# Optimization experiments

Hardware: AMD Instinct MI355X
Metric: run time of the kernel (lower is better)

The kernel has to match this reference:

```python
import jax, jax.numpy as jnp
import numpy as np
from jax import lax
import math

D_MODEL = 768
EXPAND = 2
D_INNER = EXPAND * D_MODEL          # 1536 (= d_ssm since d_ssm=None)
D_STATE = 128
HEADDIM = 64
NHEADS = D_INNER // HEADDIM         # 24
D_CONV = 4
NGROUPS = 1
CONV_DIM = D_INNER + 2 * NGROUPS * D_STATE            # 1792
D_IN_PROJ = 2 * D_INNER + 2 * NGROUPS * D_STATE + NHEADS  # d_mlp = 0
BATCH, SEQLEN = 2, 2048
EPS = 1e-5


def setup_inputs() -> dict:
    key = jax.random.key(0)
    ks = jax.random.split(key, 8)
    u = jax.random.normal(ks[0], (BATCH, SEQLEN, D_MODEL), dtype=jnp.float32)
    in_proj_w = jax.random.normal(ks[1], (D_IN_PROJ, D_MODEL), dtype=jnp.float32) / math.sqrt(D_MODEL)
    conv_w = jax.random.uniform(ks[2], (CONV_DIM, D_CONV), dtype=jnp.float32, minval=-0.5, maxval=0.5)
    conv_b = jnp.zeros((CONV_DIM,), dtype=jnp.float32)
    # dt_bias = inverse-softplus of dt sampled log-uniform in [1e-3, 1e-1]
    dt = jnp.exp(jax.random.uniform(ks[3], (NHEADS,)) * (math.log(0.1) - math.log(0.001)) + math.log(0.001))
    dt_bias = dt + jnp.log(-jnp.expm1(-dt))
    A_log = jnp.log(jax.random.uniform(ks[4], (NHEADS,), minval=1.0, maxval=16.0))
    D = jnp.ones((NHEADS,), dtype=jnp.float32)
    norm_w = jnp.ones((D_INNER,), dtype=jnp.float32)
    out_proj_w = jax.random.normal(ks[5], (D_MODEL, D_INNER), dtype=jnp.float32) / math.sqrt(D_INNER)
    return {"u": u, "in_proj_w": in_proj_w, "conv_w": conv_w, "conv_b": conv_b,
            "dt_bias": dt_bias, "A_log": A_log, "D": D, "norm_w": norm_w,
            "out_proj_w": out_proj_w}


def _mamba2_forward(u, in_proj_w, conv_w, conv_b, dt_bias, A_log, D, norm_w, out_proj_w):
    b, l, _ = u.shape
    zxbcdt = u @ in_proj_w.T                                   # [b,l,D_IN_PROJ]
    z = zxbcdt[..., :D_INNER]                                  # [b,l,d_ssm]
    xBC = zxbcdt[..., D_INNER:D_INNER + CONV_DIM]              # [b,l,conv_dim]
    dt = zxbcdt[..., D_INNER + CONV_DIM:]                      # [b,l,h]

    # causal depthwise conv1d (pad d_conv-1 left == torch pad both + truncate tail)
    xBC_t = xBC.transpose(0, 2, 1)                             # [b,c,l]
    conv_out = lax.conv_general_dilated(
        xBC_t, conv_w[:, None, :], window_strides=(1,),
        padding=[(D_CONV - 1, 0)], feature_group_count=CONV_DIM,
        dimension_numbers=("NCH", "OIH", "NCH"))
    xBC = jax.nn.silu(conv_out + conv_b[None, :, None]).transpose(0, 2, 1)  # [b,l,c]

    x = xBC[..., :D_INNER].reshape(b, l, NHEADS, HEADDIM)      # [b,l,h,p]
    B = xBC[..., D_INNER:D_INNER + D_STATE]                    # [b,l,n]
    C = xBC[..., D_INNER + D_STATE:]                           # [b,l,n]

    A = -jnp.exp(A_log)                                        # [h]
    dt_dis = jax.nn.softplus(dt + dt_bias)                     # [b,l,h]  (dt_limit=(0,inf) -> no-op clamp)
    dA = jnp.exp(dt_dis * A)                                   # [b,l,h]

    def step(state, inp):
        dA_t, dt_t, B_t, x_t, C_t = inp
        dBx = jnp.einsum("bh,bn,bhp->bhpn", dt_t, B_t, x_t)    # [b,h,p,n]
        state = lax.stop_gradient(state * dA_t[:, :, None, None] + dBx)  # matches torch .detach()
        y_t = jnp.einsum("bhpn,bn->bhp", state, C_t)
        return state, y_t

    xs = (dA.transpose(1, 0, 2), dt_dis.transpose(1, 0, 2),
          B.transpose(1, 0, 2), x.transpose(1, 0, 2, 3), C.transpose(1, 0, 2))
    state0 = jnp.zeros((b, NHEADS, HEADDIM, D_STATE), dtype=u.dtype)
    _, ys = lax.scan(step, state0, xs)                         # [l,b,h,p]
    y = ys.transpose(1, 0, 2, 3) + x * D[None, None, :, None]  # D skip (per-head)
    y = y.reshape(b, l, D_INNER)

    # gated RMSNorm (norm_before_gate=False, group_size = d_ssm)
    yz = y * jax.nn.silu(z)
    y = yz * lax.rsqrt(jnp.mean(yz * yz, axis=-1, keepdims=True) + EPS) * norm_w

    return y @ out_proj_w.T                                    # [b,l,d_model]


def reference(u, in_proj_w, conv_w, conv_b, dt_bias, A_log, D, norm_w, out_proj_w):
    return _mamba2_forward(u, in_proj_w, conv_w, conv_b, dt_bias, A_log, D, norm_w, out_proj_w)
```

## Files before the change

### kernel.cpp

```cpp
#include <hip/hip_runtime.h>
#include <hip/hip_bf16.h>
#include <math.h>

#define D_MODEL   768
#define D_INNER   1536
#define D_STATE   128
#define HEADDIM   64
#define NHEADS    24
#define D_CONV    4
#define CONV_DIM  1792
#define D_IN_PROJ 3352
#define BATCH     2
#define SEQLEN    2048
#define NROWS     (BATCH*SEQLEN)
#define EPS       1e-5f

#define NCHUNK    16
#define CHUNK     128
#define STATE_SZ  (HEADDIM*D_STATE)

#define N1_PAD    3456
#define LDST      136
#define H72       72

typedef __bf16 bf16x8 __attribute__((ext_vector_type(8)));
typedef float  f32x4  __attribute__((ext_vector_type(4)));
typedef short  s16x8  __attribute__((ext_vector_type(8)));

__device__ __forceinline__ short f2b(float f) {
    unsigned u = __float_as_uint(f);
    unsigned r = (u + 0x7FFFu + ((u >> 16) & 1u)) >> 16;
    return (short)r;
}
__device__ __forceinline__ float b2f(short s) {
    return __uint_as_float(((unsigned)(unsigned short)s) << 16);
}

__global__ __launch_bounds__(256) void gemm_bf16_kernel(
    const short* __restrict__ A, const short* __restrict__ W,
    short* __restrict__ C, int K, int Nreal, int NT)
{
    __shared__ short smem[2][2][128][32];
    int flat = blockIdx.x;
    int swz  = (flat & 7) * (gridDim.x >> 3) + (flat >> 3);
    const int m0 = (swz / NT) * 128;
    const int n0 = (swz % NT) * 128;
    const int tid  = threadIdx.x;
    const int lane = tid & 63;
    const int wid  = tid >> 6;
    const int wm = wid >> 1, wn = wid & 1;
    const int lr = lane & 15;
    const int kg = lane >> 4;

    f32x4 acc[4][4];
    #pragma unroll
    for (int i = 0; i < 4; ++i)
        #pragma unroll
        for (int j = 0; j < 4; ++j)
            acc[i][j] = (f32x4){0.f, 0.f, 0.f, 0.f};

    const int srow = (lane >> 2);
    const int scol = (lane & 3) * 8;

    auto STAGE = [&](int buf, int k0) {
        #pragma unroll
        for (int it = 0; it < 2; ++it) {
            int r = wid * 32 + it * 16;
            const short* ga = A + (size_t)(m0 + r + srow) * K + k0 + scol;
            const short* gw = W + (size_t)(n0 + r + srow) * K + k0 + scol;
            __builtin_amdgcn_global_load_lds(
                (const __attribute__((address_space(1))) void*)ga,
                (__attribute__((address_space(3))) void*)&smem[buf][0][r][0], 16, 0, 0);
            __builtin_amdgcn_global_load_lds(
                (const __attribute__((address_space(1))) void*)gw,
                (__attribute__((address_space(3))) void*)&smem[buf][1][r][0], 16, 0, 0);
        }
    };
    auto COMPUTE = [&](int buf) {
        bf16x8 af[4], bf[4];
        #pragma unroll
        for (int i = 0; i < 4; ++i)
            af[i] = *(const bf16x8*)&smem[buf][0][wm * 64 + i * 16 + lr][kg * 8];
        #pragma unroll
        for (int j = 0; j < 4; ++j)
            bf[j] = *(const bf16x8*)&smem[buf][1][wn * 64 + j * 16 + lr][kg * 8];
        #pragma unroll
        for (int i = 0; i < 4; ++i)
            #pragma unroll
            for (int j = 0; j < 4; ++j)
                acc[i][j] = __builtin_amdgcn_mfma_f32_16x16x32_bf16(af[i], bf[j], acc[i][j], 0, 0, 0);
    };

    const int nt = K >> 5;
    STAGE(0, 0);
    __syncthreads();
    int cur = 0;
    for (int t = 0; t < nt - 1; ++t) {
        STAGE(cur ^ 1, (t + 1) << 5);
        COMPUTE(cur);
        __syncthreads();
        cur ^= 1;
    }
    COMPUTE(cur);

    __syncthreads();
    short* eb = &smem[0][0][0][0];
    #pragma unroll
    for (int i = 0; i < 4; ++i)
        #pragma unroll
        for (int j = 0; j < 4; ++j)
            #pragma unroll
            for (int r = 0; r < 4; ++r) {
                int row = wm * 64 + i * 16 + kg * 4 + r;
                int col = wn * 64 + j * 16 + lr;
                eb[row * 128 + col] = f2b(acc[i][j][r]);
            }
    __syncthreads();
    #pragma unroll
    for (int ch = 0; ch < 8; ++ch) {
        int cidx = ch * 256 + tid;
        int row  = cidx >> 4;
        int cp   = cidx & 15;
        int ncol = n0 + cp * 8;
        if (ncol < Nreal)
            *(s16x8*)(C + (size_t)(m0 + row) * Nreal + ncol) =
                *(const s16x8*)(eb + row * 128 + cp * 8);
    }
}

__global__ __launch_bounds__(256) void gemm_bf16_n64_kernel(
    const short* __restrict__ A, const short* __restrict__ W,
    float* __restrict__ C, int K, int N, int NT)
{
    __shared__ short As[2][128][32];
    __shared__ short Ws[2][64][32];
    int flat = blockIdx.x;
    int swz  = (flat & 7) * (gridDim.x >> 3) + (flat >> 3);
    const int m0 = (swz / NT) * 128;
    const int n0 = (swz % NT) * 64;
    const int tid  = threadIdx.x;
    const int lane = tid & 63;
    const int wid  = tid >> 6;
    const int lr = lane & 15;
    const int kg = lane >> 4;

    f32x4 acc[2][4];
    #pragma unroll
    for (int i = 0; i < 2; ++i)
        #pragma unroll
        for (int j = 0; j < 4; ++j)
            acc[i][j] = (f32x4){0.f, 0.f, 0.f, 0.f};

    const int srow = (lane >> 2);
    const int scol = (lane & 3) * 8;

    auto STAGE = [&](int buf, int k0) {
        #pragma unroll
        for (int it = 0; it < 2; ++it) {
            int r = wid * 32 + it * 16;
            const short* ga = A + (size_t)(m0 + r + srow) * K + k0 + scol;
            __builtin_amdgcn_global_load_lds(
                (const __attribute__((address_space(1))) void*)ga,
                (__attribute__((address_space(3))) void*)&As[buf][r][0], 16, 0, 0);
        }
        int r2 = wid * 16;
        const short* gw = W + (size_t)(n0 + r2 + srow) * K + k0 + scol;
        __builtin_amdgcn_global_load_lds(
            (const __attribute__((address_space(1))) void*)gw,
            (__attribute__((address_space(3))) void*)&Ws[buf][r2][0], 16, 0, 0);
    };
    auto COMPUTE = [&](int buf) {
        bf16x8 af[2], bf[4];
        #pragma unroll
        for (int i = 0; i < 2; ++i)
            af[i] = *(const bf16x8*)&As[buf][wid * 32 + i * 16 + lr][kg * 8];
        #pragma unroll
        for (int j = 0; j < 4; ++j)
            bf[j] = *(const bf16x8*)&Ws[buf][j * 16 + lr][kg * 8];
        #pragma unroll
        for (int i = 0; i < 2; ++i)
            #pragma unroll
            for (int j = 0; j < 4; ++j)
                acc[i][j] = __builtin_amdgcn_mfma_f32_16x16x32_bf16(af[i], bf[j], acc[i][j], 0, 0, 0);
    };

    const int nt = K >> 5;
    STAGE(0, 0);
    __syncthreads();
    int cur = 0;
    for (int t = 0; t < nt - 1; ++t) {
        STAGE(cur ^ 1, (t + 1) << 5);
        COMPUTE(cur);
        __syncthreads();
        cur ^= 1;
    }
    COMPUTE(cur);

    #pragma unroll
    for (int i = 0; i < 2; ++i) {
        int mrow = m0 + wid * 32 + i * 16 + kg * 4;
        #pragma unroll
        for (int j = 0; j < 4; ++j) {
            int ncol = n0 + j * 16 + lr;
            #pragma unroll
            for (int r = 0; r < 4; ++r)
                C[(size_t)(mrow + r) * N + ncol] = acc[i][j][r];
        }
    }
}

#define N4_U   (NROWS*D_MODEL/4)
#define N4_W1  (N1_PAD*D_MODEL/4)
#define N4_W2  (D_MODEL*D_INNER/4)
__global__ __launch_bounds__(256) void fused_cast_kernel(
    const float* __restrict__ u, const float* __restrict__ w1,
    const float* __restrict__ w2,
    short* __restrict__ ub, short* __restrict__ w1b, short* __restrict__ w2b)
{
    int i = blockIdx.x * 256 + threadIdx.x;
    size_t off;
    if (i < N4_U) {
        off = (size_t)i * 4;
        float4 v = *(const float4*)(u + off);
        *(short4*)(ub + off) = make_short4(f2b(v.x), f2b(v.y), f2b(v.z), f2b(v.w));
    } else if (i < N4_U + N4_W1) {
        int j = i - N4_U;
        off = (size_t)j * 4;
        int row = (int)(off / D_MODEL);
        float4 v = make_float4(0.f, 0.f, 0.f, 0.f);
        if (row < D_IN_PROJ) v = *(const float4*)(w1 + off);
        *(short4*)(w1b + off) = make_short4(f2b(v.x), f2b(v.y), f2b(v.z), f2b(v.w));
    } else if (i < N4_U + N4_W1 + N4_W2) {
        int j = i - N4_U - N4_W1;
        off = (size_t)j * 4;
        float4 v = *(const float4*)(w2 + off);
        *(short4*)(w2b + off) = make_short4(f2b(v.x), f2b(v.y), f2b(v.z), f2b(v.w));
    }
}

#define NG      (CONV_DIM/8)
#define CONVB   (NROWS*NG/256)
#define DTB     (NROWS*NHEADS/256)
__global__ __launch_bounds__(256) void conv_dt_kernel(
    const short* __restrict__ zxb, short* __restrict__ cob,
    const float* __restrict__ cw, const float* __restrict__ cb,
    const float* __restrict__ dt_bias, const float* __restrict__ A_log,
    float* __restrict__ dtb, float* __restrict__ dta)
{
    if (blockIdx.x < CONVB) {
        int idx = blockIdx.x * 256 + threadIdx.x;
        int g = idx % NG;
        int r = idx / NG;
        int c0 = g * 8;
        int l = r & (SEQLEN - 1);

        float4 w[8];
        #pragma unroll
        for (int e = 0; e < 8; ++e)
            w[e] = *(const float4*)(cw + (size_t)(c0 + e) * 4);

        float acc[8];
        #pragma unroll
        for (int e = 0; e < 8; ++e) acc[e] = cb[c0 + e];

        #pragma unroll
        for (int tap = 0; tap < 4; ++tap) {
            if (l - 3 + tap >= 0) {
                s16x8 v = *(const s16x8*)(zxb + (size_t)(r - 3 + tap) * D_IN_PROJ + D_INNER + c0);
                #pragma unroll
                for (int e = 0; e < 8; ++e) {
                    float we = (tap == 0) ? w[e].x : (tap == 1) ? w[e].y : (tap == 2) ? w[e].z : w[e].w;
                    acc[e] = fmaf(b2f(v[e]), we, acc[e]);
                }
            }
        }
        s16x8 o;
        #pragma unroll
        for (int e = 0; e < 8; ++e)
            o[e] = f2b(acc[e] / (1.f + expf(-acc[e])));
        *(s16x8*)(cob + (size_t)r * CONV_DIM + c0) = o;
    } else {
        int idx = (blockIdx.x - CONVB) * 256 + threadIdx.x;
        int r = idx / NHEADS, h = idx - r * NHEADS;
        float x = b2f(zxb[(size_t)r * D_IN_PROJ + (D_INNER + CONV_DIM) + h]) + dt_bias[h];
        float sp = (x > 20.f) ? x : log1pf(expf(x));
        float A  = -expf(A_log[h]);
        dtb[idx] = sp;
        dta[idx] = sp * A;
    }
}

__global__ __launch_bounds__(512) void ssd_states(
    const short* __restrict__ co, const float* __restrict__ dtb,
    const float* __restrict__ dta, short* __restrict__ sstate,
    float* __restrict__ cumWend, float* __restrict__ clgbuf)
{
    __shared__ short lds[26112];
    __shared__ float clg[128];
    __shared__ float dts[128];

    int t = blockIdx.x;
    int c = t & 15;
    int hb = t >> 4;
    int h = hb % NHEADS;
    int b = hb / NHEADS;
    const int R0 = b * SEQLEN + c * CHUNK;
    const int tid  = threadIdx.x;
    const int lane = tid & 63;
    const int wid  = tid >> 6;
    const int lr = lane & 15;
    const int kg = lane >> 4;
    const short* cobase = co + (size_t)R0 * CONV_DIM;

    if (tid < 128) {
        clg[tid] = dta[(size_t)(R0 + tid) * NHEADS + h];
        dts[tid] = dtb[(size_t)(R0 + tid) * NHEADS + h];
    }
    __syncthreads();
    for (int off = 1; off < 128; off <<= 1) {
        float v = 0.f;
        if (tid < 128 && tid >= off) v = clg[tid - off];
        __syncthreads();
        if (tid < 128) clg[tid] += v;
        __syncthreads();
    }
    const float clgE = clg[127];
    if (tid < 128)
        clgbuf[((size_t)(b * NHEADS + h)) * SEQLEN + c * CHUNK + tid] = clg[tid];
    if (tid == 127)
        cumWend[(b * NHEADS + h) * NCHUNK + c] = __expf(clgE);

    short* Bt = lds;
    short* Xt = lds + 128 * LDST;
    {
        int r = tid >> 2, q = tid & 3;
        float dtv  = dts[r];
        float wstr = __expf(clgE - clg[r]);
        const short* xr = cobase + (size_t)r * CONV_DIM + h * HEADDIM + q * 16;
        s16x8 xv0 = *(const s16x8*)xr;
        s16x8 xv1 = *(const s16x8*)(xr + 8);
        #pragma unroll
        for (int e = 0; e < 8; ++e) {
            Xt[(q * 16 + e) * LDST + r]     = f2b(b2f(xv0[e]) * dtv);
            Xt[(q * 16 + 8 + e) * LDST + r] = f2b(b2f(xv1[e]) * dtv);
        }
        const short* br = cobase + (size_t)r * CONV_DIM + D_INNER + q * 32;
        #pragma unroll
        for (int i = 0; i < 4; ++i) {
            s16x8 bv = *(const s16x8*)(br + i * 8);
            #pragma unroll
            for (int e = 0; e < 8; ++e)
                Bt[(q * 32 + i * 8 + e) * LDST + r] = f2b(b2f(bv[e]) * wstr);
        }
    }
    __syncthreads();

    f32x4 acc[4];
    #pragma unroll
    for (int i = 0; i < 4; ++i) acc[i] = (f32x4){0.f, 0.f, 0.f, 0.f};
    #pragma unroll
    for (int kk = 0; kk < 4; ++kk) {
        bf16x8 af[4], bf;
        #pragma unroll
        for (int i = 0; i < 4; ++i)
            af[i] = *(const bf16x8*)(Xt + (i * 16 + lr) * LDST + kk * 32 + kg * 8);
        bf = *(const bf16x8*)(Bt + (wid * 16 + lr) * LDST + kk * 32 + kg * 8);
        #pragma unroll
        for (int i = 0; i < 4; ++i)
            acc[i] = __builtin_amdgcn_mfma_f32_16x16x32_bf16(af[i], bf, acc[i], 0, 0, 0);
    }
    __syncthreads();

    short* yt2 = lds;
    #pragma unroll
    for (int i = 0; i < 4; ++i)
        #pragma unroll
        for (int r = 0; r < 4; ++r) {
            int p = i * 16 + kg * 4 + r;
            int n = wid * 16 + lr;
            yt2[p * LDST + n] = f2b(acc[i][r]);
        }
    __syncthreads();
    short* sbase = sstate + (((size_t)(b * NHEADS + h)) * NCHUNK + c) * STATE_SZ;
    #pragma unroll
    for (int k = 0; k < 2; ++k) {
        int idx = tid * 2 + k;
        int row = idx >> 4;
        int cp  = idx & 15;
        *(s16x8*)(sbase + row * D_STATE + cp * 8) =
            *(const s16x8*)(yt2 + row * LDST + cp * 8);
    }
}

__global__ __launch_bounds__(128) void scan_chunk_prefix(
    const float* __restrict__ cumWend, short* __restrict__ sstate)
{
    int blk = blockIdx.x;
    int piece = blk & 7;
    int bh = blk >> 3;
    int tid = threadIdx.x;
    short* base = sstate + (size_t)bh * NCHUNK * STATE_SZ + piece * 1024 + tid * 8;
    const float* cw = cumWend + (size_t)bh * NCHUNK;
    float run[8];
    #pragma unroll
    for (int e = 0; e < 8; ++e) run[e] = 0.f;
    for (int c = 0; c < NCHUNK; ++c) {
        float Ac = cw[c];
        short* ptr = base + (size_t)c * STATE_SZ;
        s16x8 loc = *(s16x8*)ptr;
        s16x8 st;
        #pragma unroll
        for (int e = 0; e < 8; ++e) st[e] = f2b(run[e]);
        *(s16x8*)ptr = st;
        #pragma unroll
        for (int e = 0; e < 8; ++e)
            run[e] = fmaf(Ac, run[e], b2f(loc[e]));
    }
}

__global__ __launch_bounds__(512) void ssd_y(
    const short* __restrict__ co, const float* __restrict__ dtb,
    const float* __restrict__ clgbuf, const short* __restrict__ sstate,
    const float* __restrict__ Dvec, short* __restrict__ ybuf)
{
    __shared__ short lds[26112];
    __shared__ float clg[128];
    __shared__ float dts[128];

    int t = blockIdx.x;
    int c = t & 15;
    int hb = t >> 4;
    int h = hb % NHEADS;
    int b = hb / NHEADS;
    const int R0 = b * SEQLEN + c * CHUNK;
    const int tid  = threadIdx.x;
    const int lane = tid & 63;
    const int wid  = tid >> 6;
    const int lr = lane & 15;
    const int kg = lane >> 4;
    const short* cobase = co + (size_t)R0 * CONV_DIM;

    if (tid < 128) {
        size_t o = ((size_t)(b * NHEADS + h)) * SEQLEN + c * CHUNK + tid;
        clg[tid] = clgbuf[o];
        dts[tid] = dtb[(size_t)(R0 + tid) * NHEADS + h];
    }
    __syncthreads();

    short* CsH = lds;
    short* BsH = lds + 128 * H72;
    short* SnH = lds + 256 * H72;
    const int wmS = wid >> 2, wnS = wid & 3;
    const int wm  = wid >> 1, wn  = wid & 1;
    const short* sinit = sstate + (((size_t)(b * NHEADS + h)) * NCHUNK + c) * STATE_SZ;

    f32x4 accS[4][2];
    f32x4 accY2[2][2];
    #pragma unroll
    for (int i = 0; i < 4; ++i)
        #pragma unroll
        for (int j = 0; j < 2; ++j)
            accS[i][j] = (f32x4){0.f, 0.f, 0.f, 0.f};
    #pragma unroll
    for (int i = 0; i < 2; ++i)
        #pragma unroll
        for (int j = 0; j < 2; ++j)
            accY2[i][j] = (f32x4){0.f, 0.f, 0.f, 0.f};

    for (int kh = 0; kh < 2; ++kh) {
        {
            int r = tid >> 2, q = tid & 3;
            const short* cr = cobase + (size_t)r * CONV_DIM + (D_INNER + D_STATE) + kh * 64 + q * 16;
            const short* br = cobase + (size_t)r * CONV_DIM + D_INNER + kh * 64 + q * 16;
            *(s16x8*)(CsH + r * H72 + q * 16)     = *(const s16x8*)cr;
            *(s16x8*)(CsH + r * H72 + q * 16 + 8) = *(const s16x8*)(cr + 8);
            *(s16x8*)(BsH + r * H72 + q * 16)     = *(const s16x8*)br;
            *(s16x8*)(BsH + r * H72 + q * 16 + 8) = *(const s16x8*)(br + 8);
            int rp = tid >> 3, qp = tid & 7;
            *(s16x8*)(SnH + rp * H72 + qp * 8) =
                *(const s16x8*)(sinit + (size_t)rp * D_STATE + kh * 64 + qp * 8);
        }
        __syncthreads();
        #pragma unroll
        for (int kk = 0; kk < 2; ++kk) {
            bf16x8 af[4], bf[2];
            #pragma unroll
            for (int i = 0; i < 4; ++i)
                af[i] = *(const bf16x8*)(CsH + (wmS * 64 + i * 16 + lr) * H72 + kk * 32 + kg * 8);
            #pragma unroll
            for (int j = 0; j < 2; ++j)
                bf[j] = *(const bf16x8*)(BsH + (wnS * 32 + j * 16 + lr) * H72 + kk * 32 + kg * 8);
            #pragma unroll
            for (int i = 0; i < 4; ++i)
                #pragma unroll
                for (int j = 0; j < 2; ++j)
                    accS[i][j] = __builtin_amdgcn_mfma_f32_16x16x32_bf16(af[i], bf[j], accS[i][j], 0, 0, 0);
            bf16x8 af2[2], bf2[2];
            #pragma unroll
            for (int i = 0; i < 2; ++i)
                af2[i] = *(const bf16x8*)(CsH + (wm * 32 + i * 16 + lr) * H72 + kk * 32 + kg * 8);
            #pragma unroll
            for (int j = 0; j < 2; ++j)
                bf2[j] = *(const bf16x8*)(SnH + (wn * 32 + j * 16 + lr) * H72 + kk * 32 + kg * 8);
            #pragma unroll
            for (int i = 0; i < 2; ++i)
                #pragma unroll
                for (int j = 0; j < 2; ++j)
                    accY2[i][j] = __builtin_amdgcn_mfma_f32_16x16x32_bf16(af2[i], bf2[j], accY2[i][j], 0, 0, 0);
        }
        __syncthreads();
    }

    short* Ps = lds;
    short* Xt = lds + 128 * LDST;
    #pragma unroll
    for (int i = 0; i < 4; ++i)
        #pragma unroll
        for (int j = 0; j < 2; ++j)
            #pragma unroll
            for (int r = 0; r < 4; ++r) {
                int l  = wmS * 64 + i * 16 + kg * 4 + r;
                int lp = wnS * 32 + j * 16 + lr;
                float w = (lp <= l) ? __expf(clg[l] - clg[lp]) : 0.f;
                Ps[l * LDST + lp] = f2b(accS[i][j][r] * w);
            }
    if (tid < 256) {
        int r = tid >> 1, q = tid & 1;
        const short* xr = cobase + (size_t)r * CONV_DIM + h * HEADDIM + q * 32;
        float dtv = dts[r];
        #pragma unroll
        for (int i = 0; i < 4; ++i) {
            s16x8 xv = *(const s16x8*)(xr + i * 8);
            #pragma unroll
            for (int e = 0; e < 8; ++e)
                Xt[(q * 32 + i * 8 + e) * LDST + r] = f2b(b2f(xv[e]) * dtv);
        }
    }
    __syncthreads();

    f32x4 acc1[2][2];
    #pragma unroll
    for (int i = 0; i < 2; ++i)
        #pragma unroll
        for (int j = 0; j < 2; ++j)
            acc1[i][j] = (f32x4){0.f, 0.f, 0.f, 0.f};
    #pragma unroll
    for (int kk = 0; kk < 4; ++kk) {
        bf16x8 af[2], bf[2];
        #pragma unroll
        for (int i = 0; i < 2; ++i)
            af[i] = *(const bf16x8*)(Ps + (wm * 32 + i * 16 + lr) * LDST + kk * 32 + kg * 8);
        #pragma unroll
        for (int j = 0; j < 2; ++j)
            bf[j] = *(const bf16x8*)(Xt + (wn * 32 + j * 16 + lr) * LDST + kk * 32 + kg * 8);
        #pragma unroll
        for (int i = 0; i < 2; ++i)
            #pragma unroll
            for (int j = 0; j < 2; ++j)
                acc1[i][j] = __builtin_amdgcn_mfma_f32_16x16x32_bf16(af[i], bf[j], acc1[i][j], 0, 0, 0);
    }
    __syncthreads();

    short* yt = lds;
    const float Dh = Dvec[h];
    #pragma unroll
    for (int i = 0; i < 2; ++i)
        #pragma unroll
        for (int j = 0; j < 2; ++j)
            #pragma unroll
            for (int r = 0; r < 4; ++r) {
                int l = wm * 32 + i * 16 + kg * 4 + r;
                int p = wn * 32 + j * 16 + lr;
                float cw = __expf(clg[l]);
                float xval = b2f(cobase[(size_t)l * CONV_DIM + h * HEADDIM + p]);
                yt[l * H72 + p] = f2b(acc1[i][j][r] + cw * accY2[i][j][r] + Dh * xval);
            }
    __syncthreads();
    #pragma unroll
    for (int k = 0; k < 2; ++k) {
        int idx = tid * 2 + k;
        int row = idx >> 3;
        int cp  = idx & 7;
        *(s16x8*)(ybuf + (size_t)(R0 + row) * D_INNER + h * HEADDIM + cp * 8) =
            *(const s16x8*)(yt + row * H72 + cp * 8);
    }
}

__global__ __launch_bounds__(192) void gate_norm_kernel(
    const short* __restrict__ zxb, const short* __restrict__ ybuf,
    const float* __restrict__ norm_w, short* __restrict__ yn)
{
    int r = blockIdx.x;
    int c0 = threadIdx.x * 8;
    s16x8 zv = *(const s16x8*)(zxb + (size_t)r * D_IN_PROJ + c0);
    s16x8 yv = *(const s16x8*)(ybuf + (size_t)r * D_INNER + c0);
    float vals[8];
    float ss = 0.f;
    #pragma unroll
    for (int e = 0; e < 8; ++e) {
        float z = b2f(zv[e]);
        float y = b2f(yv[e]);
        float v = y * (z / (1.f + expf(-z)));
        vals[e] = v;
        ss = fmaf(v, v, ss);
    }
    ss += __shfl_xor(ss, 1);
    ss += __shfl_xor(ss, 2);
    ss += __shfl_xor(ss, 4);
    ss += __shfl_xor(ss, 8);
    ss += __shfl_xor(ss, 16);
    ss += __shfl_xor(ss, 32);
    __shared__ float red[3];
    if ((threadIdx.x & 63) == 0) red[threadIdx.x >> 6] = ss;
    __syncthreads();
    float tot = red[0] + red[1] + red[2];
    float scale = rsqrtf(tot / (float)D_INNER + EPS);
    float4 nw0 = *(const float4*)(norm_w + c0);
    float4 nw1 = *(const float4*)(norm_w + c0 + 4);
    const float nw[8] = {nw0.x, nw0.y, nw0.z, nw0.w, nw1.x, nw1.y, nw1.z, nw1.w};
    s16x8 o;
    #pragma unroll
    for (int e = 0; e < 8; ++e)
        o[e] = f2b(vals[e] * scale * nw[e]);
    *(s16x8*)(yn + (size_t)r * D_INNER + c0) = o;
}

extern "C" void kernel_launch(void* const* d_in, const int* in_sizes, int n_in,
                              void* d_out, int out_size, void* d_ws, size_t ws_size,
                              hipStream_t stream) {
    const float* u          = (const float*)d_in[0];
    const float* in_proj_w  = (const float*)d_in[1];
    const float* conv_w     = (const float*)d_in[2];
    const float* conv_b     = (const float*)d_in[3];
    const float* dt_bias    = (const float*)d_in[4];
    const float* A_log      = (const float*)d_in[5];
    const float* Dvec       = (const float*)d_in[6];
    const float* norm_w     = (const float*)d_in[7];
    const float* out_proj_w = (const float*)d_in[8];
    float* out = (float*)d_out;

    short* zxb    = (short*)d_ws;
    short* cob    = zxb + (size_t)NROWS * D_IN_PROJ;
    float* dtb    = (float*)(cob + (size_t)NROWS * CONV_DIM);
    float* dta    = dtb  + (size_t)NROWS * NHEADS;
    short* ybuf   = (short*)(dta + (size_t)NROWS * NHEADS);
    short* sstate = ybuf + (size_t)NROWS * D_INNER;
    float* cumWend= (float*)(sstate + (size_t)BATCH*NHEADS*NCHUNK*STATE_SZ);
    float* clgbuf = cumWend + BATCH*NHEADS*NCHUNK;
    short* w2b    = (short*)(clgbuf + (size_t)BATCH*NHEADS*SEQLEN);

    short* ub  = sstate;
    short* w1b = ub + (size_t)NROWS * D_MODEL;
    short* ynb = sstate;

    {
        int total = N4_U + N4_W1 + N4_W2;
        fused_cast_kernel<<<(total + 255)/256, 256, 0, stream>>>(u, in_proj_w, out_proj_w, ub, w1b, w2b);
    }
    gemm_bf16_kernel<<<(NROWS/128)*(N1_PAD/128), 256, 0, stream>>>(ub, w1b, zxb, D_MODEL, D_IN_PROJ, N1_PAD/128);
    conv_dt_kernel<<<CONVB + DTB, 256, 0, stream>>>(zxb, cob, conv_w, conv_b, dt_bias, A_log, dtb, dta);
    ssd_states<<<BATCH*NHEADS*NCHUNK, 512, 0, stream>>>(cob, dtb, dta, sstate, cumWend, clgbuf);
    scan_chunk_prefix<<<BATCH*NHEADS*8, 128, 0, stream>>>(cumWend, sstate);
    ssd_y<<<BATCH*NHEADS*NCHUNK, 512, 0, stream>>>(cob, dtb, clgbuf, sstate, Dvec, ybuf);
    gate_norm_kernel<<<NROWS, 192, 0, stream>>>(zxb, ybuf, norm_w, ynb);
    gemm_bf16_n64_kernel<<<(NROWS/128)*(D_MODEL/64), 256, 0, stream>>>(ynb, w2b, out, D_INNER, D_MODEL, D_MODEL/64);
}
```

Baseline: 235.1 us.

## Fuse causal conv, SiLU and dt softplus into SSD state and output kernels

Removes the standalone conv_dt kernel and its intermediate conv-output and dt buffers. ssd_states and ssd_y now compute the depthwise causal conv plus SiLU and the dt softplus on the fly from the in-projection output. The D-skip term is recovered from the dt-scaled X tile in shared memory by multiplying by 1/dt, instead of reloading x. This saves one launch and a global round trip. In exchange, B/C/x conv work is recomputed across the 24 heads, with extra reads of four taps per row and fast-math exp.

After: 333.2 us. +41.7%, slower.

```diff
diff --git a/kernel.cpp b/kernel.cpp
--- a/kernel.cpp
+++ b/kernel.cpp
@@ -34,6 +34,33 @@
 }
 __device__ __forceinline__ float b2f(short s) {
     return __uint_as_float(((unsigned)(unsigned short)s) << 16);
+}
+__device__ __forceinline__ float silu(float x) {
+    return x / (1.f + __expf(-x));
+}
+
+__device__ __forceinline__ void conv8(
+    const short* __restrict__ zrow,
+    int seqpos, int cc,
+    const float* __restrict__ cw, const float* __restrict__ cb,
+    float acc8[8])
+{
+    float4 wv[8];
+    #pragma unroll
+    for (int e = 0; e < 8; ++e) wv[e] = *(const float4*)(cw + (size_t)(cc + e) * 4);
+    #pragma unroll
+    for (int e = 0; e < 8; ++e) acc8[e] = cb[cc + e];
+    #pragma unroll
+    for (int t = 0; t < 4; ++t) {
+        if (seqpos - 3 + t >= 0) {
+            s16x8 v = *(const s16x8*)(zrow + (ptrdiff_t)(t - 3) * D_IN_PROJ + D_INNER + cc);
+            #pragma unroll
+            for (int e = 0; e < 8; ++e) {
+                float we = (t == 0) ? wv[e].x : (t == 1) ? wv[e].y : (t == 2) ? wv[e].z : wv[e].w;
+                acc8[e] = fmaf(b2f(v[e]), we, acc8[e]);
+            }
+        }
+    }
 }
 
 __global__ __launch_bounds__(256) void gemm_bf16_kernel(
@@ -238,62 +265,12 @@
     }
 }
 
-#define NG      (CONV_DIM/8)
-#define CONVB   (NROWS*NG/256)
-#define DTB     (NROWS*NHEADS/256)
-__global__ __launch_bounds__(256) void conv_dt_kernel(
-    const short* __restrict__ zxb, short* __restrict__ cob,
+__global__ __launch_bounds__(512) void ssd_states(
+    const short* __restrict__ zxb,
     const float* __restrict__ cw, const float* __restrict__ cb,
     const float* __restrict__ dt_bias, const float* __restrict__ A_log,
-    float* __restrict__ dtb, float* __restrict__ dta)
-{
-    if (blockIdx.x < CONVB) {
-        int idx = blockIdx.x * 256 + threadIdx.x;
-        int g = idx % NG;
-        int r = idx / NG;
-        int c0 = g * 8;
-        int l = r & (SEQLEN - 1);
-
-        float4 w[8];
-        #pragma unroll
-        for (int e = 0; e < 8; ++e)
-            w[e] = *(const float4*)(cw + (size_t)(c0 + e) * 4);
-
-        float acc[8];
-        #pragma unroll
-        for (int e = 0; e < 8; ++e) acc[e] = cb[c0 + e];
-
-        #pragma unroll
-        for (int tap = 0; tap < 4; ++tap) {
-            if (l - 3 + tap >= 0) {
-                s16x8 v = *(const s16x8*)(zxb + (size_t)(r - 3 + tap) * D_IN_PROJ + D_INNER + c0);
-                #pragma unroll
-                for (int e = 0; e < 8; ++e) {
-                    float we = (tap == 0) ? w[e].x : (tap == 1) ? w[e].y : (tap == 2) ? w[e].z : w[e].w;
-                    acc[e] = fmaf(b2f(v[e]), we, acc[e]);
-                }
-            }
-        }
-        s16x8 o;
-        #pragma unroll
-        for (int e = 0; e < 8; ++e)
-            o[e] = f2b(acc[e] / (1.f + expf(-acc[e])));
-        *(s16x8*)(cob + (size_t)r * CONV_DIM + c0) = o;
-    } else {
-        int idx = (blockIdx.x - CONVB) * 256 + threadIdx.x;
-        int r = idx / NHEADS, h = idx - r * NHEADS;
-        float x = b2f(zxb[(size_t)r * D_IN_PROJ + (D_INNER + CONV_DIM) + h]) + dt_bias[h];
-        float sp = (x > 20.f) ? x : log1pf(expf(x));
-        float A  = -expf(A_log[h]);
-        dtb[idx] = sp;
-        dta[idx] = sp * A;
-    }
-}
-
-__global__ __launch_bounds__(512) void ssd_states(
-    const short* __restrict__ co, const float* __restrict__ dtb,
-    const float* __restrict__ dta, short* __restrict__ sstate,
-    float* __restrict__ cumWend, float* __restrict__ clgbuf)
+    short* __restrict__ sstate, float* __restrict__ cumWend,
+    float* __restrict__ clgbuf)
 {
     __shared__ short lds[26112];
     __shared__ float clg[128];
@@ -310,11 +287,12 @@
     const int wid  = tid >> 6;
     const int lr = lane & 15;
     const int kg = lane >> 4;
-    const short* cobase = co + (size_t)R0 * CONV_DIM;
 
     if (tid < 128) {
-        clg[tid] = dta[(size_t)(R0 + tid) * NHEADS + h];
-        dts[tid] = dtb[(size_t)(R0 + tid) * NHEADS + h];
+        float x = b2f(zxb[(size_t)(R0 + tid) * D_IN_PROJ + (D_INNER + CONV_DIM) + h]) + dt_bias[h];
+        float sp = (x > 20.f) ? x : log1pf(__expf(x));
+        dts[tid] = sp;
+        clg[tid] = sp * (-__expf(A_log[h]));
     }
     __syncthreads();
     for (int off = 1; off < 128; off <<= 1) {
@@ -334,23 +312,27 @@
     short* Xt = lds + 128 * LDST;
     {
         int r = tid >> 2, q = tid & 3;
+        int seqpos = c * CHUNK + r;
+        const short* zrow = zxb + (size_t)(R0 + r) * D_IN_PROJ;
         float dtv  = dts[r];
         float wstr = __expf(clgE - clg[r]);
-        const short* xr = cobase + (size_t)r * CONV_DIM + h * HEADDIM + q * 16;
-        s16x8 xv0 = *(const s16x8*)xr;
-        s16x8 xv1 = *(const s16x8*)(xr + 8);
-        #pragma unroll
-        for (int e = 0; e < 8; ++e) {
-            Xt[(q * 16 + e) * LDST + r]     = f2b(b2f(xv0[e]) * dtv);
-            Xt[(q * 16 + 8 + e) * LDST + r] = f2b(b2f(xv1[e]) * dtv);
-        }
-        const short* br = cobase + (size_t)r * CONV_DIM + D_INNER + q * 32;
-        #pragma unroll
-        for (int i = 0; i < 4; ++i) {
-            s16x8 bv = *(const s16x8*)(br + i * 8);
+        #pragma unroll
+        for (int g8 = 0; g8 < 2; ++g8) {
+            int cc = h * HEADDIM + q * 16 + g8 * 8;
+            float a8[8];
+            conv8(zrow, seqpos, cc, cw, cb, a8);
             #pragma unroll
             for (int e = 0; e < 8; ++e)
-                Bt[(q * 32 + i * 8 + e) * LDST + r] = f2b(b2f(bv[e]) * wstr);
+                Xt[(q * 16 + g8 * 8 + e) * LDST + r] = f2b(silu(a8[e]) * dtv);
+        }
+        #pragma unroll
+        for (int g8 = 0; g8 < 4; ++g8) {
+            int cc = D_INNER + q * 32 + g8 * 8;
+            float a8[8];
+            conv8(zrow, seqpos, cc, cw, cb, a8);
+            #pragma unroll
+            for (int e = 0; e < 8; ++e)
+                Bt[(q * 32 + g8 * 8 + e) * LDST + r] = f2b(silu(a8[e]) * wstr);
         }
     }
     __syncthreads();
@@ -419,13 +401,16 @@
 }
 
 __global__ __launch_bounds__(512) void ssd_y(
-    const short* __restrict__ co, const float* __restrict__ dtb,
+    const short* __restrict__ zxb,
+    const float* __restrict__ cw, const float* __restrict__ cb,
+    const float* __restrict__ dt_bias,
     const float* __restrict__ clgbuf, const short* __restrict__ sstate,
     const float* __restrict__ Dvec, short* __restrict__ ybuf)
 {
     __shared__ short lds[26112];
     __shared__ float clg[128];
     __shared__ float dts[128];
+    __shared__ float idts[128];
 
     int t = blockIdx.x;
     int c = t & 15;
@@ -438,12 +423,14 @@
     const int wid  = tid >> 6;
     const int lr = lane & 15;
     const int kg = lane >> 4;
-    const short* cobase = co + (size_t)R0 * CONV_DIM;
 
     if (tid < 128) {
         size_t o = ((size_t)(b * NHEADS + h)) * SEQLEN + c * CHUNK + tid;
         clg[tid] = clgbuf[o];
-        dts[tid] = dtb[(size_t)(R0 + tid) * NHEADS + h];
+        float x = b2f(zxb[(size_t)(R0 + tid) * D_IN_PROJ + (D_INNER + CONV_DIM) + h]) + dt_bias[h];
+        float sp = (x > 20.f) ? x : log1pf(__expf(x));
+        dts[tid]  = sp;
+        idts[tid] = 1.f / sp;
     }
     __syncthreads();
 
@@ -470,12 +457,24 @@
     for (int kh = 0; kh < 2; ++kh) {
         {
             int r = tid >> 2, q = tid & 3;
-            const short* cr = cobase + (size_t)r * CONV_DIM + (D_INNER + D_STATE) + kh * 64 + q * 16;
-            const short* br = cobase + (size_t)r * CONV_DIM + D_INNER + kh * 64 + q * 16;
-            *(s16x8*)(CsH + r * H72 + q * 16)     = *(const s16x8*)cr;
-            *(s16x8*)(CsH + r * H72 + q * 16 + 8) = *(const s16x8*)(cr + 8);
-            *(s16x8*)(BsH + r * H72 + q * 16)     = *(const s16x8*)br;
-            *(s16x8*)(BsH + r * H72 + q * 16 + 8) = *(const s16x8*)(br + 8);
+            int seqpos = c * CHUNK + r;
+            const short* zrow = zxb + (size_t)(R0 + r) * D_IN_PROJ;
+            #pragma unroll
+            for (int g8 = 0; g8 < 2; ++g8) {
+                int ccC = D_INNER + D_STATE + kh * 64 + q * 16 + g8 * 8;
+                float a8[8];
+                conv8(zrow, seqpos, ccC, cw, cb, a8);
+                s16x8 o;
+                #pragma unroll
+                for (int e = 0; e < 8; ++e) o[e] = f2b(silu(a8[e]));
+                *(s16x8*)(CsH + r * H72 + q * 16 + g8 * 8) = o;
+
+                int ccB = D_INNER + kh * 64 + q * 16 + g8 * 8;
+                conv8(zrow, seqpos, ccB, cw, cb, a8);
+                #pragma unroll
+                for (int e = 0; e < 8; ++e) o[e] = f2b(silu(a8[e]));
+                *(s16x8*)(BsH + r * H72 + q * 16 + g8 * 8) = o;
+            }
             int rp = tid >> 3, qp = tid & 7;
             *(s16x8*)(SnH + rp * H72 + qp * 8) =
                 *(const s16x8*)(sinit + (size_t)rp * D_STATE + kh * 64 + qp * 8);
@@ -526,14 +525,17 @@
             }
     if (tid < 256) {
         int r = tid >> 1, q = tid & 1;
-        const short* xr = cobase + (size_t)r * CONV_DIM + h * HEADDIM + q * 32;
+        int seqpos = c * CHUNK + r;
+        const short* zrow = zxb + (size_t)(R0 + r) * D_IN_PROJ;
         float dtv = dts[r];
         #pragma unroll
-        for (int i = 0; i < 4; ++i) {
-            s16x8 xv = *(const s16x8*)(xr + i * 8);
+        for (int g8 = 0; g8 < 4; ++g8) {
+            int cc = h * HEADDIM + q * 32 + g8 * 8;
+            float a8[8];
+            conv8(zrow, seqpos, cc, cw, cb, a8);
             #pragma unroll
             for (int e = 0; e < 8; ++e)
-                Xt[(q * 32 + i * 8 + e) * LDST + r] = f2b(b2f(xv[e]) * dtv);
+                Xt[(q * 32 + g8 * 8 + e) * LDST + r] = f2b(silu(a8[e]) * dtv);
         }
     }
     __syncthreads();
@@ -571,9 +573,9 @@
             for (int r = 0; r < 4; ++r) {
                 int l = wm * 32 + i * 16 + kg * 4 + r;
                 int p = wn * 32 + j * 16 + lr;
-                float cw = __expf(clg[l]);
-                float xval = b2f(cobase[(size_t)l * CONV_DIM + h * HEADDIM + p]);
-                yt[l * H72 + p] = f2b(acc1[i][j][r] + cw * accY2[i][j][r] + Dh * xval);
+                float cwv = __expf(clg[l]);
+                float xval = b2f(Xt[p * LDST + l]) * idts[l];
+                yt[l * H72 + p] = f2b(acc1[i][j][r] + cwv * accY2[i][j][r] + Dh * xval);
             }
     __syncthreads();
     #pragma unroll
@@ -600,7 +602,7 @@
     for (int e = 0; e < 8; ++e) {
         float z = b2f(zv[e]);
         float y = b2f(yv[e]);
-        float v = y * (z / (1.f + expf(-z)));
+        float v = y * (z / (1.f + __expf(-z)));
         vals[e] = v;
         ss = fmaf(v, v, ss);
     }
@@ -640,10 +642,7 @@
     float* out = (float*)d_out;
 
     short* zxb    = (short*)d_ws;
-    short* cob    = zxb + (size_t)NROWS * D_IN_PROJ;
-    float* dtb    = (float*)(cob + (size_t)NROWS * CONV_DIM);
-    float* dta    = dtb  + (size_t)NROWS * NHEADS;
-    short* ybuf   = (short*)(dta + (size_t)NROWS * NHEADS);
+    short* ybuf   = zxb + (size_t)NROWS * D_IN_PROJ;
     short* sstate = ybuf + (size_t)NROWS * D_INNER;
     float* cumWend= (float*)(sstate + (size_t)BATCH*NHEADS*NCHUNK*STATE_SZ);
     float* clgbuf = cumWend + BATCH*NHEADS*NCHUNK;
@@ -658,10 +657,9 @@
         fused_cast_kernel<<<(total + 255)/256, 256, 0, stream>>>(u, in_proj_w, out_proj_w, ub, w1b, w2b);
     }
     gemm_bf16_kernel<<<(NROWS/128)*(N1_PAD/128), 256, 0, stream>>>(ub, w1b, zxb, D_MODEL, D_IN_PROJ, N1_PAD/128);
-    conv_dt_kernel<<<CONVB + DTB, 256, 0, stream>>>(zxb, cob, conv_w, conv_b, dt_bias, A_log, dtb, dta);
-    ssd_states<<<BATCH*NHEADS*NCHUNK, 512, 0, stream>>>(cob, dtb, dta, sstate, cumWend, clgbuf);
+    ssd_states<<<BATCH*NHEADS*NCHUNK, 512, 0, stream>>>(zxb, conv_w, conv_b, dt_bias, A_log, sstate, cumWend, clgbuf);
     scan_chunk_prefix<<<BATCH*NHEADS*8, 128, 0, stream>>>(cumWend, sstate);
-    ssd_y<<<BATCH*NHEADS*NCHUNK, 512, 0, stream>>>(cob, dtb, clgbuf, sstate, Dvec, ybuf);
+    ssd_y<<<BATCH*NHEADS*NCHUNK, 512, 0, stream>>>(zxb, conv_w, conv_b, dt_bias, clgbuf, sstate, Dvec, ybuf);
     gate_norm_kernel<<<NROWS, 192, 0, stream>>>(zxb, ybuf, norm_w, ynb);
     gemm_bf16_n64_kernel<<<(NROWS/128)*(D_MODEL/64), 256, 0, stream>>>(ynb, w2b, out, D_INNER, D_MODEL, D_MODEL/64);
 }
```
